# Kernel optimization log

Hardware: AMD Instinct MI355X
Metric: run time of the kernel (lower is better)

Reference implementation:

```python
import jax, jax.numpy as jnp
import numpy as np

B, S, D, H, K = 2, 2048, 1024, 16, 16


def setup_inputs() -> dict:
    key = jax.random.key(0)
    ks = jax.random.split(key, 8)
    s = 0.02
    def w(k, shape):
        return s * jax.random.normal(k, shape, jnp.float32)
    return {
        "x": jax.random.normal(ks[0], (B, S, D), jnp.float32),
        "Wq": w(ks[1], (D, D)), "bq": jnp.zeros((D,), jnp.float32),
        "Wk": w(ks[2], (D, D)), "bk": jnp.zeros((D,), jnp.float32),
        "Wv": w(ks[3], (D, D)), "bv": jnp.zeros((D,), jnp.float32),
        "Wo": w(ks[4], (D, D)), "bo": jnp.zeros((D,), jnp.float32),
        "Ws1": w(ks[5], (D, D // 2)), "bs1": jnp.zeros((D // 2,), jnp.float32),
        "Ws2": w(ks[6], (D // 2, 1)), "bs2": jnp.zeros((1,), jnp.float32),
    }


def reference(x, Wq, bq, Wk, bk, Wv, bv, Wo, bo, Ws1, bs1, Ws2, bs2):
    Bx, Sx, Dx = x.shape
    Dh = Dx // H
    # QKV projections -> [B, H, S, Dh]
    q = (x @ Wq + bq).reshape(Bx, Sx, H, Dh).transpose(0, 2, 1, 3)
    k = (x @ Wk + bk).reshape(Bx, Sx, H, Dh).transpose(0, 2, 1, 3)
    v = (x @ Wv + bv).reshape(Bx, Sx, H, Dh).transpose(0, 2, 1, 3)
    scores = jnp.einsum('bhqd,bhkd->bhqk', q, k) / np.float32(np.sqrt(Dh))
    # Lightning-indexer importance: [B, S]; identical across heads, so compute once.
    imp = jax.nn.sigmoid(jax.nn.relu(x @ Ws1 + bs1) @ Ws2 + bs2)[..., 0]
    _, idx = jax.lax.top_k(imp, K)  # [B, K]
    sel = jnp.zeros((Bx, Sx), bool).at[jnp.arange(Bx)[:, None], idx].set(True)
    # sparse mask: position (i, j) kept if row i OR column j is a top-k token
    m2 = sel[:, :, None] | sel[:, None, :]  # [B, S, S]
    masked = jnp.where(m2[:, None, :, :], scores, -jnp.inf)
    w = jax.nn.softmax(masked, axis=-1)
    att = jnp.einsum('bhqk,bhkd->bhqd', w, v).transpose(0, 2, 1, 3).reshape(Bx, Sx, Dx)
    return att @ Wo + bo
```

## Files before the change

### kernel.cpp

```cpp
#include <hip/hip_runtime.h>
#include <math.h>

constexpr int Bb = 2, Ss = 2048, Dd = 1024, Hh = 16, Kk = 16;
constexpr float DELTA = 0.02f;

typedef __bf16 bf16x8 __attribute__((ext_vector_type(8)));
typedef __bf16 bf16x4 __attribute__((ext_vector_type(4)));
typedef float  f32x4  __attribute__((ext_vector_type(4)));

__device__ __forceinline__ void gld_lds16(const void* g, void* l) {
    __builtin_amdgcn_global_load_lds(
        (const __attribute__((address_space(1))) unsigned int*)g,
        (__attribute__((address_space(3))) unsigned int*)l, 16, 0, 0);
}

__global__ void __launch_bounds__(256) gemm_qkv_ind(
    const __bf16* __restrict__ xb, const __bf16* __restrict__ WqkvT,
    const __bf16* __restrict__ W1Th,
    const float* __restrict__ bq, const float* __restrict__ bk,
    const float* __restrict__ bv,
    __bf16* __restrict__ qb, __bf16* __restrict__ kb, __bf16* __restrict__ vb,
    const float* __restrict__ bs1, const float* __restrict__ Ws2,
    float* __restrict__ imp)
{
    __shared__ __bf16 As[128 * 32];
    __shared__ __bf16 Bs[128 * 32];

    const int bid  = blockIdx.x;
    const int cb   = bid % 28;
    const int bm   = (bid / 28) * 128;
    const int t    = threadIdx.x;
    const int wave = t >> 6;
    const int lane = t & 63;
    const int fr   = lane & 15;
    const int fq   = lane >> 4;
    const int K    = Dd;
    const bool ind = (cb >= 24);

    const __bf16* BT = ind ? (W1Th + (size_t)(cb - 24) * 128 * 1024)
                           : (WqkvT + (size_t)cb * 128 * 1024);

    const int wm = (wave & 1) * 64;
    const int wn = (wave >> 1) * 64;

    f32x4 acc[4][4] = {};

    for (int k0 = 0; k0 < K; k0 += 32) {
        #pragma unroll
        for (int l = 0; l < 2; ++l) {
            int c = l * 256 + t;
            int row = c >> 2, seg = (c & 3) ^ (row & 3);
            gld_lds16(xb + (size_t)(bm + row) * K + k0 + seg * 8,
                      As + (size_t)(l * 256 + wave * 64) * 8);
            gld_lds16(BT + (size_t)row * K + k0 + seg * 8,
                      Bs + (size_t)(l * 256 + wave * 64) * 8);
        }
        __syncthreads();

        bf16x8 af[4], bf[4];
        #pragma unroll
        for (int i = 0; i < 4; ++i) {
            int row = wm + i * 16 + fr;
            af[i] = *(const bf16x8*)(As + row * 32 + ((fq ^ (row & 3)) * 8));
        }
        #pragma unroll
        for (int j = 0; j < 4; ++j) {
            int row = wn + j * 16 + fr;
            bf[j] = *(const bf16x8*)(Bs + row * 32 + ((fq ^ (row & 3)) * 8));
        }
        #pragma unroll
        for (int i = 0; i < 4; ++i)
            #pragma unroll
            for (int j = 0; j < 4; ++j)
                acc[i][j] = __builtin_amdgcn_mfma_f32_16x16x32_bf16(af[i], bf[j], acc[i][j], 0, 0, 0);
        __syncthreads();
    }

    const int cr = (lane >> 4) * 4;
    const int cc = lane & 15;

    if (!ind) {
        const int zone = cb >> 3;
        const int cl0  = cb * 128 - zone * 1024;
        const float* bias = (zone == 0) ? bq : (zone == 1) ? bk : bv;
        __bf16*      C    = (zone == 0) ? qb : (zone == 1) ? kb : vb;
        #pragma unroll
        for (int j = 0; j < 4; ++j) {
            int col = cl0 + wn + j * 16 + cc;
            float bb = bias[col];
            #pragma unroll
            for (int i = 0; i < 4; ++i) {
                #pragma unroll
                for (int r = 0; r < 4; ++r)
                    C[(size_t)(bm + wm + i * 16 + cr + r) * Dd + col] =
                        (__bf16)(acc[i][j][r] + bb);
            }
        }
    } else {
        const int hc0 = (cb - 24) * 128;
        float bb[4], w2[4];
        #pragma unroll
        for (int j = 0; j < 4; ++j) {
            int col = hc0 + wn + j * 16 + cc;
            bb[j] = bs1[col];
            w2[j] = Ws2[col];
        }
        #pragma unroll
        for (int i = 0; i < 4; ++i) {
            #pragma unroll
            for (int r = 0; r < 4; ++r) {
                float vsum = 0.f;
                #pragma unroll
                for (int j = 0; j < 4; ++j)
                    vsum += fmaxf(acc[i][j][r] + bb[j], 0.f) * w2[j];
                #pragma unroll
                for (int off = 8; off > 0; off >>= 1)
                    vsum += __shfl_xor(vsum, off, 16);
                if (cc == 0)
                    atomicAdd(imp + (bm + wm + i * 16 + cr + r), vsum);
            }
        }
    }
}

__global__ void __launch_bounds__(256) gemm_out(
    const __bf16* __restrict__ A, const __bf16* __restrict__ BT,
    const float* __restrict__ bias, float* __restrict__ C, int M, int N, int K)
{
    __shared__ __bf16 As[64 * 64];
    __shared__ __bf16 Bs[128 * 64];

    const int t    = threadIdx.x;
    const int wave = t >> 6;
    const int lane = t & 63;
    const int bm   = blockIdx.y * 64;
    const int bn   = blockIdx.x * 128;
    const int wm   = (wave & 1) * 32;
    const int wn   = (wave >> 1) * 64;
    const int fr   = lane & 15;
    const int fq   = lane >> 4;

    f32x4 acc[2][4] = {};

    for (int k0 = 0; k0 < K; k0 += 64) {
        #pragma unroll
        for (int l = 0; l < 2; ++l) {
            int c = l * 256 + t;
            int row = c >> 3, seg = (c & 7) ^ (row & 7);
            gld_lds16(A + (size_t)(bm + row) * K + k0 + seg * 8,
                      As + (size_t)(l * 256 + wave * 64) * 8);
        }
        #pragma unroll
        for (int l = 0; l < 4; ++l) {
            int c = l * 256 + t;
            int row = c >> 3, seg = (c & 7) ^ (row & 7);
            gld_lds16(BT + (size_t)(bn + row) * K + k0 + seg * 8,
                      Bs + (size_t)(l * 256 + wave * 64) * 8);
        }
        __syncthreads();

        #pragma unroll
        for (int s = 0; s < 2; ++s) {
            bf16x8 af[2], bf[4];
            #pragma unroll
            for (int i = 0; i < 2; ++i) {
                int row = wm + i * 16 + fr;
                af[i] = *(const bf16x8*)(As + row * 64 + (((s * 4 + fq) ^ (row & 7)) * 8));
            }
            #pragma unroll
            for (int j = 0; j < 4; ++j) {
                int row = wn + j * 16 + fr;
                bf[j] = *(const bf16x8*)(Bs + row * 64 + (((s * 4 + fq) ^ (row & 7)) * 8));
            }
            #pragma unroll
            for (int i = 0; i < 2; ++i)
                #pragma unroll
                for (int j = 0; j < 4; ++j)
                    acc[i][j] = __builtin_amdgcn_mfma_f32_16x16x32_bf16(af[i], bf[j], acc[i][j], 0, 0, 0);
        }
        __syncthreads();
    }

    const int cr = (lane >> 4) * 4;
    const int cc = lane & 15;
    #pragma unroll
    for (int j = 0; j < 4; ++j) {
        int col = bn + wn + j * 16 + cc;
        float bb = bias[col];
        #pragma unroll
        for (int i = 0; i < 2; ++i) {
            #pragma unroll
            for (int r = 0; r < 4; ++r)
                C[(size_t)(bm + wm + i * 16 + cr + r) * N + col] = acc[i][j][r] + bb;
        }
    }
}

__global__ void __launch_bounds__(256) prep_kernel(
    const float* __restrict__ x, __bf16* __restrict__ xb,
    float* __restrict__ imp, float* __restrict__ oacc,
    float* __restrict__ lsum, float* __restrict__ hbuf,
    int* __restrict__ ccount,
    const float* __restrict__ W0, const float* __restrict__ W1,
    const float* __restrict__ W2, const float* __restrict__ W3,
    __bf16* __restrict__ WqkvT, __bf16* __restrict__ WoT,
    const float* __restrict__ Ws1, __bf16* __restrict__ Th)
{
    __shared__ float tile[32][33];
    const int bid = blockIdx.x;

    if (bid < 4096) {
        int i = bid * 256 + threadIdx.x;
        if (i < Bb * Ss) imp[i] = 0.f;
        if (i < Bb * Hh * Kk * 64) oacc[i] = 0.f;
        if (i < Bb * Hh * Kk) lsum[i] = 0.f;
        if (i < Bb * 64 * 512) hbuf[i] = 0.f;
        if (i < Bb) ccount[i] = 0;
        float4 v = ((const float4*)x)[i];
        bf16x4 h = { (__bf16)v.x, (__bf16)v.y, (__bf16)v.z, (__bf16)v.w };
        ((bf16x4*)xb)[i] = h;
        return;
    }

    int tid = bid - 4096;
    int z   = tid >> 10;
    int rem = tid & 1023;
    int n0  = (rem & 31) * 32;
    int k0  = (rem >> 5) * 32;
    int tx = threadIdx.x & 31, ty = threadIdx.x >> 5;

    if (z < 4) {
        const float* W = (z == 0) ? W0 : (z == 1) ? W1 : (z == 2) ? W2 : W3;
        __bf16*      T = (z < 3) ? (WqkvT + (size_t)z * 1024 * 1024) : WoT;
        #pragma unroll
        for (int i = 0; i < 32; i += 8)
            tile[ty + i][tx] = W[(size_t)(k0 + ty + i) * 1024 + n0 + tx];
        __syncthreads();
        #pragma unroll
        for (int i = 0; i < 32; i += 8)
            T[(size_t)(n0 + ty + i) * 1024 + k0 + tx] = (__bf16)tile[tx][ty + i];
    } else {
        if (n0 >= 512) return;
        #pragma unroll
        for (int i = 0; i < 32; i += 8)
            tile[ty + i][tx] = Ws1[(size_t)(k0 + ty + i) * 512 + n0 + tx];
        __syncthreads();
        #pragma unroll
        for (int i = 0; i < 32; i += 8)
            Th[(size_t)(n0 + ty + i) * 1024 + k0 + tx] = (__bf16)tile[tx][ty + i];
    }
}

__global__ void __launch_bounds__(256) topk_cand(
    const float* __restrict__ imp, int* __restrict__ cand_idx,
    int* __restrict__ ccount)
{
    int b = blockIdx.x;
    int t = threadIdx.x;
    int wave = t >> 6, lane = t & 63;
    __shared__ float vals[Ss];
    __shared__ float sv[4];
    __shared__ int   si[4];
    __shared__ float thr_s;
    __shared__ int   cnt_s;

    for (int j = t; j < Ss; j += 256) vals[j] = imp[b * Ss + j];
    __syncthreads();

    for (int it = 0; it < Kk; ++it) {
        float best = -1e30f; int bidx = 0x7fffffff;
        for (int j = t; j < Ss; j += 256) {
            float v = vals[j];
            if (v > best || (v == best && j < bidx)) { best = v; bidx = j; }
        }
        #pragma unroll
        for (int off = 32; off > 0; off >>= 1) {
            float ov = __shfl_xor(best, off, 64);
            int   oi = __shfl_xor(bidx, off, 64);
            if (ov > best || (ov == best && oi < bidx)) { best = ov; bidx = oi; }
        }
        if (lane == 0) { sv[wave] = best; si[wave] = bidx; }
        __syncthreads();
        if (t == 0) {
            float bv = sv[0]; int br = si[0];
            #pragma unroll
            for (int w = 1; w < 4; ++w)
                if (sv[w] > bv || (sv[w] == bv && si[w] < br)) { bv = sv[w]; br = si[w]; }
            cand_idx[b * 64 + it] = br;
            vals[br] = -1e30f;
            if (it == Kk - 1) { thr_s = bv - DELTA; cnt_s = Kk; }
        }
        __syncthreads();
    }

    float thr = thr_s;
    for (int j = t; j < Ss; j += 256) {
        if (vals[j] > thr) {
            int p = atomicAdd(&cnt_s, 1);
            if (p < 64) cand_idx[b * 64 + p] = j;
        }
    }
    __syncthreads();
    if (t == 0) ccount[b] = min(cnt_s, 64);
}

__global__ void __launch_bounds__(256) rescore_h(
    const float* __restrict__ x, const float* __restrict__ Ws1,
    const int* __restrict__ cand_idx, const int* __restrict__ ccount,
    float* __restrict__ hbuf)
{
    const int c = blockIdx.x, kc = blockIdx.y, b = blockIdx.z;
    if (c >= ccount[b]) return;
    const int row = cand_idx[b * 64 + c];
    const int t = threadIdx.x;
    const int k0 = kc * 64;

    __shared__ float xs[64];
    if (t < 16)
        ((float4*)xs)[t] = ((const float4*)(x + ((size_t)(b * Ss + row)) * Dd + k0))[t];
    __syncthreads();

    float a0 = 0.f, a1 = 0.f;
    const float* W = Ws1 + (size_t)k0 * 512;
    #pragma unroll 16
    for (int kk = 0; kk < 64; ++kk) {
        float xv = xs[kk];
        a0 = fmaf(xv, W[kk * 512 + t], a0);
        a1 = fmaf(xv, W[kk * 512 + t + 256], a1);
    }
    float* hb = hbuf + ((size_t)(b * 64 + c)) * 512;
    atomicAdd(hb + t, a0);
    atomicAdd(hb + t + 256, a1);
}

__global__ void __launch_bounds__(256) rescore_fin(
    const float* __restrict__ hbuf, const float* __restrict__ bs1,
    const float* __restrict__ Ws2, const int* __restrict__ ccount,
    float* __restrict__ candz)
{
    const int c = blockIdx.x, b = blockIdx.y;
    if (c >= ccount[b]) return;
    const int t = threadIdx.x;
    __shared__ float red[256];
    const float* hb = hbuf + ((size_t)(b * 64 + c)) * 512;
    float zp = fmaxf(hb[t] + bs1[t], 0.f) * Ws2[t]
             + fmaxf(hb[t + 256] + bs1[t + 256], 0.f) * Ws2[t + 256];
    red[t] = zp;
    __syncthreads();
    for (int off = 128; off > 0; off >>= 1) {
        if (t < off) red[t] += red[t + off];
        __syncthreads();
    }
    if (t == 0) candz[b * 64 + c] = red[0];
}

__global__ void __launch_bounds__(64) select_k(
    const float* __restrict__ candz, const int* __restrict__ cand_idx,
    const int* __restrict__ ccount, int* __restrict__ sel_idx)
{
    const int b = blockIdx.x, t = threadIdx.x;
    const int cnt = ccount[b];
    float val = (t < cnt) ? candz[b * 64 + t] : -1e30f;
    int   row = (t < cnt) ? cand_idx[b * 64 + t] : 0x7fffffff;

    for (int it = 0; it < Kk; ++it) {
        float bv = val; int br = row;
        #pragma unroll
        for (int off = 1; off < 64; off <<= 1) {
            float ov = __shfl_xor(bv, off, 64);
            int   orw = __shfl_xor(br, off, 64);
            if (ov > bv || (ov == bv && orw < br)) { bv = ov; br = orw; }
        }
        if (row == br) val = -1e30f;
        if (t == 0) sel_idx[b * Kk + it] = br;
    }
}

__global__ void __launch_bounds__(256) attn_sparse(
    const __bf16* __restrict__ q, const __bf16* __restrict__ k,
    const __bf16* __restrict__ v, const int* __restrict__ sel_idx,
    __bf16* __restrict__ att)
{
    const int b  = blockIdx.z;
    const int h  = blockIdx.y;
    const int q0 = blockIdx.x * 16;
    const int t  = threadIdx.x;

    __shared__ float KT[64][17];
    __shared__ float Vs[16][64];
    __shared__ float qsh[16][65];
    __shared__ float wsh[16][16];
    __shared__ int   sj[16];

    if (t < 16) sj[t] = sel_idx[b * Kk + t];
    __syncthreads();

    {
        int row = t >> 4, d0 = (t & 15) * 4;
        bf16x4 kv = *(const bf16x4*)(k + ((size_t)(b * Ss + sj[row])) * Dd + h * 64 + d0);
        bf16x4 vv = *(const bf16x4*)(v + ((size_t)(b * Ss + sj[row])) * Dd + h * 64 + d0);
        bf16x4 qv = *(const bf16x4*)(q + ((size_t)(b * Ss + q0 + row)) * Dd + h * 64 + d0);
        #pragma unroll
        for (int i = 0; i < 4; ++i) {
            KT[d0 + i][row]  = (float)kv[i];
            Vs[row][d0 + i]  = (float)vv[i];
            qsh[row][d0 + i] = (float)qv[i];
        }
    }
    __syncthreads();

    const int wave = t >> 6, lane = t & 63;
    const int ql = lane >> 4, j = lane & 15;
    const int qi = wave * 4 + ql;

    float s = 0.f;
    #pragma unroll
    for (int d = 0; d < 64; ++d) s = fmaf(qsh[qi][d], KT[d][j], s);
    s *= 0.125f;

    float m = s;
    #pragma unroll
    for (int off = 8; off > 0; off >>= 1) m = fmaxf(m, __shfl_xor(m, off, 16));
    float e = __expf(s - m);
    float sum = e;
    #pragma unroll
    for (int off = 8; off > 0; off >>= 1) sum += __shfl_xor(sum, off, 16);
    wsh[qi][j] = e / sum;

    #pragma unroll
    for (int q2 = 0; q2 < 4; ++q2) {
        int qq = wave * 4 + q2;
        float o = 0.f;
        #pragma unroll
        for (int jj = 0; jj < 16; ++jj)
            o = fmaf(wsh[qq][jj], Vs[jj][lane], o);
        att[((size_t)(b * Ss + q0 + qq)) * Dd + h * 64 + lane] = (__bf16)o;
    }
}

__global__ void __launch_bounds__(256) attn_dense_one(
    const __bf16* __restrict__ q, const __bf16* __restrict__ k,
    const __bf16* __restrict__ v, const int* __restrict__ sel_idx,
    float* __restrict__ lsum, float* __restrict__ oacc)
{
    const int b  = blockIdx.z, h = blockIdx.y, j0 = blockIdx.x * 128;
    const int t  = threadIdx.x;

    __shared__ float Ks[128][65];
    __shared__ float Qs[16][65];
    __shared__ float Es[16][144];

    #pragma unroll
    for (int l = 0; l < 4; ++l) {
        int c = t + 256 * l;
        int row = c >> 3, seg = c & 7;
        bf16x8 kv = *(const bf16x8*)(k + ((size_t)(b * Ss + j0 + row)) * Dd + h * 64 + seg * 8);
        #pragma unroll
        for (int e = 0; e < 8; ++e) Ks[row][seg * 8 + e] = (float)kv[e];
    }
    if (t < 128) {
        int row = t >> 3, seg = t & 7;
        int i = sel_idx[b * Kk + row];
        bf16x8 qv = *(const bf16x8*)(q + ((size_t)(b * Ss + i)) * Dd + h * 64 + seg * 8);
        #pragma unroll
        for (int e = 0; e < 8; ++e) Qs[row][seg * 8 + e] = (float)qv[e];
    }
    __syncthreads();

    const int qi = t >> 4, ks = t & 15;
    const int bhq = (b * Hh + h) * Kk + qi;
    float psum = 0.f;
    #pragma unroll
    for (int s8 = 0; s8 < 8; ++s8) {
        int j = ks + s8 * 16;
        float s = 0.f;
        #pragma unroll
        for (int d = 0; d < 64; ++d) s = fmaf(Qs[qi][d], Ks[j][d], s);
        float e = __expf(s * 0.125f);
        Es[qi][j] = e;
        psum += e;
    }
    #pragma unroll
    for (int off = 8; off > 0; off >>= 1) psum += __shfl_xor(psum, off, 16);
    if (ks == 0) atomicAdd(lsum + bhq, psum);
    __syncthreads();

    #pragma unroll
    for (int l = 0; l < 4; ++l) {
        int c = t + 256 * l;
        int row = c >> 3, seg = c & 7;
        bf16x8 vv = *(const bf16x8*)(v + ((size_t)(b * Ss + j0 + row)) * Dd + h * 64 + seg * 8);
        #pragma unroll
        for (int e = 0; e < 8; ++e) Ks[row][seg * 8 + e] = (float)vv[e];
    }
    __syncthreads();

    const int d = t & 63, qg = t >> 6;
    #pragma unroll
    for (int qq = 0; qq < 4; ++qq) {
        int qx = qg * 4 + qq;
        float o = 0.f;
        #pragma unroll 4
        for (int jj = 0; jj < 128; ++jj)
            o = fmaf(Es[qx][jj], Ks[jj][d], o);
        atomicAdd(oacc + (size_t)((b * Hh + h) * Kk + qx) * 64 + d, o);
    }
}

__global__ void __launch_bounds__(64) attn_dense_fin(
    const float* __restrict__ oacc, const float* __restrict__ lsum,
    const int* __restrict__ sel_idx, __bf16* __restrict__ att)
{
    int bid = blockIdx.x;
    int qi = bid & 15, h = (bid >> 4) & 15, b = bid >> 8;
    int bhq = (b * Hh + h) * Kk + qi;
    int i = sel_idx[b * Kk + qi];
    float val = oacc[(size_t)bhq * 64 + threadIdx.x] / lsum[bhq];
    att[((size_t)(b * Ss + i)) * Dd + h * 64 + threadIdx.x] = (__bf16)val;
}

extern "C" void kernel_launch(void* const* d_in, const int* in_sizes, int n_in,
                              void* d_out, int out_size, void* d_ws, size_t ws_size,
                              hipStream_t stream)
{
    const float* x   = (const float*)d_in[0];
    const float* Wq  = (const float*)d_in[1];
    const float* bq  = (const float*)d_in[2];
    const float* Wk  = (const float*)d_in[3];
    const float* bk  = (const float*)d_in[4];
    const float* Wv  = (const float*)d_in[5];
    const float* bv  = (const float*)d_in[6];
    const float* Wo  = (const float*)d_in[7];
    const float* bo  = (const float*)d_in[8];
    const float* Ws1 = (const float*)d_in[9];
    const float* bs1 = (const float*)d_in[10];
    const float* Ws2 = (const float*)d_in[11];
    float* out = (float*)d_out;

    const size_t MSD = (size_t)Bb * Ss * Dd;
    const int M = Bb * Ss;

    char* p = (char*)d_ws;
    __bf16* qb  = (__bf16*)p; p += MSD * sizeof(__bf16);
    __bf16* kb  = (__bf16*)p; p += MSD * sizeof(__bf16);
    __bf16* vb  = (__bf16*)p; p += MSD * sizeof(__bf16);
    __bf16* att = (__bf16*)p; p += MSD * sizeof(__bf16);
    __bf16* xb  = (__bf16*)p; p += MSD * sizeof(__bf16);
    __bf16* WqkvT = (__bf16*)p; p += (size_t)3 * Dd * Dd * sizeof(__bf16);
    __bf16* WoT   = (__bf16*)p; p += (size_t)Dd * Dd * sizeof(__bf16);
    __bf16* W1Th  = (__bf16*)p; p += (size_t)512 * Dd * sizeof(__bf16);
    float* imp  = (float*)p; p += (size_t)Bb * Ss * sizeof(float);
    int* sel_idx = (int*)p; p += (size_t)Bb * Kk * sizeof(int);
    float* oacc = (float*)p; p += (size_t)Bb * Hh * Kk * 64 * sizeof(float);
    float* lsum = (float*)p; p += (size_t)Bb * Hh * Kk * sizeof(float);
    float* hbuf = (float*)p; p += (size_t)Bb * 64 * 512 * sizeof(float);
    int* ccount   = (int*)p; p += Bb * sizeof(int);
    int* cand_idx = (int*)p; p += (size_t)Bb * 64 * sizeof(int);
    float* candz  = (float*)p; p += (size_t)Bb * 64 * sizeof(float);

    prep_kernel<<<dim3(4096 + 5120), 256, 0, stream>>>(
        x, xb, imp, oacc, lsum, hbuf, ccount,
        Wq, Wk, Wv, Wo, WqkvT, WoT, Ws1, W1Th);
    gemm_qkv_ind<<<dim3(896), 256, 0, stream>>>(
        xb, WqkvT, W1Th, bq, bk, bv, qb, kb, vb, bs1, Ws2, imp);
    topk_cand<<<dim3(Bb), 256, 0, stream>>>(imp, cand_idx, ccount);
    rescore_h<<<dim3(64, 16, Bb), 256, 0, stream>>>(x, Ws1, cand_idx, ccount, hbuf);
    rescore_fin<<<dim3(64, Bb), 256, 0, stream>>>(hbuf, bs1, Ws2, ccount, candz);
    select_k<<<dim3(Bb), 64, 0, stream>>>(candz, cand_idx, ccount, sel_idx);
    attn_sparse<<<dim3(Ss / 16, Hh, Bb), 256, 0, stream>>>(qb, kb, vb, sel_idx, att);
    attn_dense_one<<<dim3(Ss / 128, Hh, Bb), 256, 0, stream>>>(qb, kb, vb, sel_idx, lsum, oacc);
    attn_dense_fin<<<dim3(Bb * Hh * Kk), 64, 0, stream>>>(oacc, lsum, sel_idx, att);
    gemm_out<<<dim3(8, 64), 256, 0, stream>>>(att, WoT, bo, out, M, Dd, Dd);
}
```

Before: 280.2 us.

## Enlarge QKV GEMM tile, widen top-k block, fuse rescore finish with selection

The QKV/indexer GEMM now uses 512-thread blocks with a 256x128 tile, so each weight tile is reused across twice as many rows and half as many blocks are launched. The XOR swizzle on the LDS layout is removed, which may bring back LDS bank conflicts on the fragment reads. Top-k candidate search now runs 1024 threads per batch, with each thread owning two fixed elements, which removes the strided scan loops. The rescore finish and top-K selection kernels are merged into one kernel, cutting one launch and the candz round trip through global memory.

Result: slower. 290.5 us (+3.7%).

```diff
diff --git a/kernel.cpp b/kernel.cpp
--- a/kernel.cpp
+++ b/kernel.cpp
@@ -14,7 +14,7 @@
         (__attribute__((address_space(3))) unsigned int*)l, 16, 0, 0);
 }
 
-__global__ void __launch_bounds__(256) gemm_qkv_ind(
+__global__ void __launch_bounds__(512) gemm_qkv_ind(
     const __bf16* __restrict__ xb, const __bf16* __restrict__ WqkvT,
     const __bf16* __restrict__ W1Th,
     const float* __restrict__ bq, const float* __restrict__ bk,
@@ -23,12 +23,12 @@
     const float* __restrict__ bs1, const float* __restrict__ Ws2,
     float* __restrict__ imp)
 {
-    __shared__ __bf16 As[128 * 32];
+    __shared__ __bf16 As[256 * 32];
     __shared__ __bf16 Bs[128 * 32];
 
     const int bid  = blockIdx.x;
     const int cb   = bid % 28;
-    const int bm   = (bid / 28) * 128;
+    const int bm   = (bid / 28) * 256;
     const int t    = threadIdx.x;
     const int wave = t >> 6;
     const int lane = t & 63;
@@ -40,34 +40,33 @@
     const __bf16* BT = ind ? (W1Th + (size_t)(cb - 24) * 128 * 1024)
                            : (WqkvT + (size_t)cb * 128 * 1024);
 
-    const int wm = (wave & 1) * 64;
-    const int wn = (wave >> 1) * 64;
+    const int wm = (wave & 3) * 64;
+    const int wn = (wave >> 2) * 64;
 
     f32x4 acc[4][4] = {};
 
     for (int k0 = 0; k0 < K; k0 += 32) {
         #pragma unroll
         for (int l = 0; l < 2; ++l) {
-            int c = l * 256 + t;
-            int row = c >> 2, seg = (c & 3) ^ (row & 3);
+            int c = l * 512 + t;
+            int row = c >> 2, seg = c & 3;
             gld_lds16(xb + (size_t)(bm + row) * K + k0 + seg * 8,
-                      As + (size_t)(l * 256 + wave * 64) * 8);
+                      As + (size_t)(l * 512 + wave * 64) * 8);
+        }
+        {
+            int row = t >> 2, seg = t & 3;
             gld_lds16(BT + (size_t)row * K + k0 + seg * 8,
-                      Bs + (size_t)(l * 256 + wave * 64) * 8);
+                      Bs + (size_t)(wave * 64) * 8);
         }
         __syncthreads();
 
         bf16x8 af[4], bf[4];
         #pragma unroll
-        for (int i = 0; i < 4; ++i) {
-            int row = wm + i * 16 + fr;
-            af[i] = *(const bf16x8*)(As + row * 32 + ((fq ^ (row & 3)) * 8));
-        }
-        #pragma unroll
-        for (int j = 0; j < 4; ++j) {
-            int row = wn + j * 16 + fr;
-            bf[j] = *(const bf16x8*)(Bs + row * 32 + ((fq ^ (row & 3)) * 8));
-        }
+        for (int i = 0; i < 4; ++i)
+            af[i] = *(const bf16x8*)(As + (wm + i * 16 + fr) * 32 + fq * 8);
+        #pragma unroll
+        for (int j = 0; j < 4; ++j)
+            bf[j] = *(const bf16x8*)(Bs + (wn + j * 16 + fr) * 32 + fq * 8);
         #pragma unroll
         for (int i = 0; i < 4; ++i)
             #pragma unroll
@@ -251,7 +250,7 @@
     }
 }
 
-__global__ void __launch_bounds__(256) topk_cand(
+__global__ void __launch_bounds__(1024) topk_cand(
     const float* __restrict__ imp, int* __restrict__ cand_idx,
     int* __restrict__ ccount)
 {
@@ -259,20 +258,19 @@
     int t = threadIdx.x;
     int wave = t >> 6, lane = t & 63;
     __shared__ float vals[Ss];
-    __shared__ float sv[4];
-    __shared__ int   si[4];
+    __shared__ float sv[16];
+    __shared__ int   si[16];
     __shared__ float thr_s;
     __shared__ int   cnt_s;
 
-    for (int j = t; j < Ss; j += 256) vals[j] = imp[b * Ss + j];
+    vals[t]        = imp[b * Ss + t];
+    vals[t + 1024] = imp[b * Ss + t + 1024];
     __syncthreads();
 
     for (int it = 0; it < Kk; ++it) {
-        float best = -1e30f; int bidx = 0x7fffffff;
-        for (int j = t; j < Ss; j += 256) {
-            float v = vals[j];
-            if (v > best || (v == best && j < bidx)) { best = v; bidx = j; }
-        }
+        float v0 = vals[t], v1 = vals[t + 1024];
+        float best = v0; int bidx = t;
+        if (v1 > best) { best = v1; bidx = t + 1024; }
         #pragma unroll
         for (int off = 32; off > 0; off >>= 1) {
             float ov = __shfl_xor(best, off, 64);
@@ -284,7 +282,7 @@
         if (t == 0) {
             float bv = sv[0]; int br = si[0];
             #pragma unroll
-            for (int w = 1; w < 4; ++w)
+            for (int w = 1; w < 16; ++w)
                 if (sv[w] > bv || (sv[w] == bv && si[w] < br)) { bv = sv[w]; br = si[w]; }
             cand_idx[b * 64 + it] = br;
             vals[br] = -1e30f;
@@ -294,11 +292,13 @@
     }
 
     float thr = thr_s;
-    for (int j = t; j < Ss; j += 256) {
-        if (vals[j] > thr) {
-            int p = atomicAdd(&cnt_s, 1);
-            if (p < 64) cand_idx[b * 64 + p] = j;
-        }
+    if (vals[t] > thr) {
+        int p = atomicAdd(&cnt_s, 1);
+        if (p < 64) cand_idx[b * 64 + p] = t;
+    }
+    if (vals[t + 1024] > thr) {
+        int p = atomicAdd(&cnt_s, 1);
+        if (p < 64) cand_idx[b * 64 + p] = t + 1024;
     }
     __syncthreads();
     if (t == 0) ccount[b] = min(cnt_s, 64);
@@ -333,46 +333,46 @@
     atomicAdd(hb + t + 256, a1);
 }
 
-__global__ void __launch_bounds__(256) rescore_fin(
+__global__ void __launch_bounds__(256) rescore_sel(
     const float* __restrict__ hbuf, const float* __restrict__ bs1,
-    const float* __restrict__ Ws2, const int* __restrict__ ccount,
-    float* __restrict__ candz)
-{
-    const int c = blockIdx.x, b = blockIdx.y;
-    if (c >= ccount[b]) return;
-    const int t = threadIdx.x;
-    __shared__ float red[256];
-    const float* hb = hbuf + ((size_t)(b * 64 + c)) * 512;
-    float zp = fmaxf(hb[t] + bs1[t], 0.f) * Ws2[t]
-             + fmaxf(hb[t + 256] + bs1[t + 256], 0.f) * Ws2[t + 256];
-    red[t] = zp;
-    __syncthreads();
-    for (int off = 128; off > 0; off >>= 1) {
-        if (t < off) red[t] += red[t + off];
-        __syncthreads();
-    }
-    if (t == 0) candz[b * 64 + c] = red[0];
-}
-
-__global__ void __launch_bounds__(64) select_k(
-    const float* __restrict__ candz, const int* __restrict__ cand_idx,
+    const float* __restrict__ Ws2, const int* __restrict__ cand_idx,
     const int* __restrict__ ccount, int* __restrict__ sel_idx)
 {
     const int b = blockIdx.x, t = threadIdx.x;
+    const int wave = t >> 6, lane = t & 63;
+    __shared__ float zv[64];
+    __shared__ float sv[4];
     const int cnt = ccount[b];
-    float val = (t < cnt) ? candz[b * 64 + t] : -1e30f;
-    int   row = (t < cnt) ? cand_idx[b * 64 + t] : 0x7fffffff;
-
-    for (int it = 0; it < Kk; ++it) {
-        float bv = val; int br = row;
-        #pragma unroll
-        for (int off = 1; off < 64; off <<= 1) {
-            float ov = __shfl_xor(bv, off, 64);
-            int   orw = __shfl_xor(br, off, 64);
-            if (ov > bv || (ov == bv && orw < br)) { bv = ov; br = orw; }
-        }
-        if (row == br) val = -1e30f;
-        if (t == 0) sel_idx[b * Kk + it] = br;
+
+    const float b0 = bs1[t],       b1 = bs1[t + 256];
+    const float w0 = Ws2[t],       w1 = Ws2[t + 256];
+
+    for (int c = 0; c < cnt; ++c) {
+        const float* hb = hbuf + ((size_t)(b * 64 + c)) * 512;
+        float zp = fmaxf(hb[t] + b0, 0.f) * w0
+                 + fmaxf(hb[t + 256] + b1, 0.f) * w1;
+        #pragma unroll
+        for (int off = 32; off > 0; off >>= 1) zp += __shfl_xor(zp, off, 64);
+        if (lane == 0) sv[wave] = zp;
+        __syncthreads();
+        if (t == 0) zv[c] = (sv[0] + sv[1]) + (sv[2] + sv[3]);
+        __syncthreads();
+    }
+
+    if (t < 64) {
+        float val = (t < cnt) ? zv[t] : -1e30f;
+        int   row = (t < cnt) ? cand_idx[b * 64 + t] : 0x7fffffff;
+        for (int it = 0; it < Kk; ++it) {
+            float bv = val; int br = row;
+            #pragma unroll
+            for (int off = 1; off < 64; off <<= 1) {
+                float ov = __shfl_xor(bv, off, 64);
+                int   orw = __shfl_xor(br, off, 64);
+                if (ov > bv || (ov == bv && orw < br)) { bv = ov; br = orw; }
+            }
+            if (row == br) val = -1e30f;
+            if (t == 0) sel_idx[b * Kk + it] = br;
+        }
     }
 }
 
@@ -556,17 +556,15 @@
     float* hbuf = (float*)p; p += (size_t)Bb * 64 * 512 * sizeof(float);
     int* ccount   = (int*)p; p += Bb * sizeof(int);
     int* cand_idx = (int*)p; p += (size_t)Bb * 64 * sizeof(int);
-    float* candz  = (float*)p; p += (size_t)Bb * 64 * sizeof(float);
 
     prep_kernel<<<dim3(4096 + 5120), 256, 0, stream>>>(
         x, xb, imp, oacc, lsum, hbuf, ccount,
         Wq, Wk, Wv, Wo, WqkvT, WoT, Ws1, W1Th);
-    gemm_qkv_ind<<<dim3(896), 256, 0, stream>>>(
+    gemm_qkv_ind<<<dim3(448), 512, 0, stream>>>(
         xb, WqkvT, W1Th, bq, bk, bv, qb, kb, vb, bs1, Ws2, imp);
-    topk_cand<<<dim3(Bb), 256, 0, stream>>>(imp, cand_idx, ccount);
+    topk_cand<<<dim3(Bb), 1024, 0, stream>>>(imp, cand_idx, ccount);
     rescore_h<<<dim3(64, 16, Bb), 256, 0, stream>>>(x, Ws1, cand_idx, ccount, hbuf);
-    rescore_fin<<<dim3(64, Bb), 256, 0, stream>>>(hbuf, bs1, Ws2, ccount, candz);
-    select_k<<<dim3(Bb), 64, 0, stream>>>(candz, cand_idx, ccount, sel_idx);
+    rescore_sel<<<dim3(Bb), 256, 0, stream>>>(hbuf, bs1, Ws2, cand_idx, ccount, sel_idx);
     attn_sparse<<<dim3(Ss / 16, Hh, Bb), 256, 0, stream>>>(qb, kb, vb, sel_idx, att);
     attn_dense_one<<<dim3(Ss / 128, Hh, Bb), 256, 0, stream>>>(qb, kb, vb, sel_idx, lsum, oacc);
     attn_dense_fin<<<dim3(Bb * Hh * Kk), 64, 0, stream>>>(oacc, lsum, sel_idx, att);
```
